# Performance work log

Hardware: AMD Instinct MI355X
Metric: run time of the kernel (lower is better)

The kernel has to match this reference:

```python
import jax, jax.numpy as jnp
import numpy as np

N = 100000      # nodes
E = 3200000     # edges (avg degree 32)
DIN, DH, DOUT = 256, 256, 64
K = 10          # propagation hops


def _uniform(key, shape, fan_in):
    b = 1.0 / np.sqrt(fan_in)
    return jax.random.uniform(key, shape, jnp.float32, -b, b)


def setup_inputs() -> dict:
    key = jax.random.key(0)
    ks = jax.random.split(key, 8)
    x = jax.random.normal(ks[0], (N, DIN), jnp.float32)
    edge_index = jax.random.randint(ks[1], (2, E), 0, N, dtype=jnp.int64)
    W1 = _uniform(ks[2], (DIN, DH), DIN)
    b1 = _uniform(ks[3], (DH,), DIN)
    W2 = _uniform(ks[4], (DH, DOUT), DH)
    b2 = _uniform(ks[5], (DOUT,), DH)
    proj_w = _uniform(ks[6], (DOUT,), DOUT)
    proj_b = _uniform(ks[7], (), DOUT)
    return {"x": x, "edge_index": edge_index, "W1": W1, "b1": b1,
            "W2": W2, "b2": b2, "proj_w": proj_w, "proj_b": proj_b}


def _gcn_norm(edge_index, num_nodes):
    # add self-loops with weight 1, symmetric normalization deg^-1/2 A deg^-1/2
    loops = jnp.arange(num_nodes, dtype=edge_index.dtype)
    row = jnp.concatenate([edge_index[0], loops])
    col = jnp.concatenate([edge_index[1], loops])
    w = jnp.ones(row.shape[0], jnp.float32)
    deg = jax.ops.segment_sum(w, col, num_segments=num_nodes)
    dinv = jnp.where(deg > 0, jax.lax.rsqrt(deg), 0.0)
    norm = dinv[row] * dinv[col]  # edge weight is 1
    return row, col, norm


def reference(x, edge_index, W1, b1, W2, b2, proj_w, proj_b):
    h = jax.nn.relu(x @ W1 + b1)
    h = h @ W2 + b2                               # [N, DOUT]
    row, col, norm = _gcn_norm(edge_index, N)
    preds = [h]
    for _ in range(K):
        h = jax.ops.segment_sum(norm[:, None] * h[row], col, num_segments=N)
        preds.append(h)
    pps = jnp.stack(preds, axis=1)                # [N, K+1, DOUT]
    score = jax.nn.sigmoid(pps @ proj_w + proj_b) # [N, K+1]
    out = jnp.einsum('nk,nkc->nc', score, pps)    # adaptive hop pooling
    return out
```

## Files before the change

kernel.cpp:

```cpp
#include <hip/hip_runtime.h>
#include <hip/hip_bf16.h>
#include <math.h>


#define WAVE 64
#define NBLK 1024

__device__ inline float bf2f(unsigned short u) {
    union { unsigned int i; float f; } v; v.i = ((unsigned int)u) << 16; return v.f;
}
__device__ inline unsigned short f2bf(float f) {
    __hip_bfloat16 b = __float2bfloat16(f);
    union { __hip_bfloat16 b; unsigned short u; } v; v.b = b; return v.u;
}

typedef __attribute__((ext_vector_type(8))) short bf16x8;
typedef __attribute__((ext_vector_type(16))) float f32x16;

__global__ void detect_kernel(const unsigned* __restrict__ e, int* __restrict__ sflag) {
    __shared__ int any;
    if (threadIdx.x == 0) any = 0;
    __syncthreads();
    unsigned nz = 0;
    int t = threadIdx.x;
    for (int i = 0; i < 8; ++i) nz |= e[(size_t)(t * 8 + i) * 2 + 1];
    if (nz) atomicOr(&any, 1);
    __syncthreads();
    if (t == 0) *sflag = any ? 1 : 2;
}

__global__ void passA_kernel(const int* __restrict__ eidx, const int* __restrict__ sflag,
                             int* __restrict__ blk_cnt, int E, int NB, int EPB) {
    __shared__ int lh[512];
    int t = threadIdx.x, blk = blockIdx.x;
    for (int i = t; i < NB; i += 256) lh[i] = 0;
    __syncthreads();
    int s = *sflag;
    int base = blk * EPB;
    int end = base + EPB; if (end > E) end = E;
    for (int e = base + t; e < end; e += 256) {
        int c = eidx[(size_t)s * (size_t)(E + e)];
        atomicAdd(&lh[c >> 8], 1);
    }
    __syncthreads();
    for (int i = t; i < NB; i += 256)
        blk_cnt[(size_t)i * NBLK + blk] = lh[i];
}

__global__ void scan1_kernel(const int* __restrict__ in, int* __restrict__ out,
                             int* __restrict__ bsums, int n) {
    __shared__ int s[256];
    int t = threadIdx.x;
    int idx = blockIdx.x * 1024 + t * 4;
    int x0 = (idx + 0 < n) ? in[idx + 0] : 0;
    int x1 = (idx + 1 < n) ? in[idx + 1] : 0;
    int x2 = (idx + 2 < n) ? in[idx + 2] : 0;
    int x3 = (idx + 3 < n) ? in[idx + 3] : 0;
    int lsum = x0 + x1 + x2 + x3;
    s[t] = lsum;
    __syncthreads();
    for (int o = 1; o < 256; o <<= 1) {
        int v = (t >= o) ? s[t - o] : 0;
        __syncthreads();
        if (t >= o) s[t] += v;
        __syncthreads();
    }
    int excl = s[t] - lsum;
    if (idx + 0 < n) out[idx + 0] = excl;
    if (idx + 1 < n) out[idx + 1] = excl + x0;
    if (idx + 2 < n) out[idx + 2] = excl + x0 + x1;
    if (idx + 3 < n) out[idx + 3] = excl + x0 + x1 + x2;
    if (t == 255) bsums[blockIdx.x] = s[255];
}

__global__ void scan2g_kernel(int* __restrict__ bsums, int nb) {
    __shared__ int part[256];
    int t = threadIdx.x;
    int v[4]; int run = 0;
    #pragma unroll
    for (int j = 0; j < 4; ++j) {
        int i = t * 4 + j;
        int x = (i < nb) ? bsums[i] : 0;
        v[j] = run; run += x;
    }
    part[t] = run;
    __syncthreads();
    for (int o = 1; o < 256; o <<= 1) {
        int x = (t >= o) ? part[t - o] : 0;
        __syncthreads();
        if (t >= o) part[t] += x;
        __syncthreads();
    }
    int excl = part[t] - run;
    #pragma unroll
    for (int j = 0; j < 4; ++j) {
        int i = t * 4 + j;
        if (i < nb) bsums[i] = excl + v[j];
    }
}

__global__ void scan3_kernel(int* __restrict__ arr, const int* __restrict__ bsums,
                             int n, int total) {
    int t = threadIdx.x;
    int idx = blockIdx.x * 1024 + t * 4;
    int add = bsums[blockIdx.x];
    #pragma unroll
    for (int i = 0; i < 4; ++i)
        if (idx + i < n) arr[idx + i] += add;
    if (blockIdx.x == 0 && t == 0) arr[n] = total;
}

__global__ void passB_kernel(const int* __restrict__ eidx, const int* __restrict__ sflag,
                             const int* __restrict__ pbase, int2* __restrict__ pairs,
                             int E, int NB, int EPB) {
    __shared__ int lcur[512];
    int t = threadIdx.x, blk = blockIdx.x;
    for (int i = t; i < NB; i += 256) lcur[i] = pbase[(size_t)i * NBLK + blk];
    __syncthreads();
    int s = *sflag;
    int base = blk * EPB;
    int end = base + EPB; if (end > E) end = E;
    for (int e = base + t; e < end; e += 256) {
        int r = eidx[(size_t)s * (size_t)e];
        int c = eidx[(size_t)s * (size_t)(E + e)];
        int pos = atomicAdd(&lcur[c >> 8], 1);
        pairs[pos] = make_int2(r, c);
    }
}

__global__ void passD_kernel(const int2* __restrict__ pairs, const int* __restrict__ pbase,
                             int* __restrict__ cnt, int N) {
    __shared__ int lcnt[256];
    int b = blockIdx.x, t = threadIdx.x;
    lcnt[t] = 0;
    __syncthreads();
    int w0 = pbase[(size_t)b * NBLK], w1 = pbase[(size_t)(b + 1) * NBLK];
    for (int i = w0 + t; i < w1; i += 256)
        atomicAdd(&lcnt[pairs[i].y & 255], 1);
    __syncthreads();
    int node = b * 256 + t;
    if (node < N) cnt[node] = lcnt[t];
}

__global__ void dinv_kernel(const int* __restrict__ cnt, float* __restrict__ dinv, int n) {
    int i = blockIdx.x * blockDim.x + threadIdx.x;
    if (i < n) dinv[i] = rsqrtf((float)(cnt[i] + 1));
}

__global__ void passC_kernel(const int2* __restrict__ pairs, const int* __restrict__ pbase,
                             const int* __restrict__ offs, int* __restrict__ csr_src,
                             int N) {
    __shared__ int lcur[256];
    int b = blockIdx.x, t = threadIdx.x;
    int node = b * 256 + t;
    lcur[t] = (node < N) ? offs[node] : 0;
    __syncthreads();
    int w0 = pbase[(size_t)b * NBLK], w1 = pbase[(size_t)(b + 1) * NBLK];
    for (int i = w0 + t; i < w1; i += 256) {
        int2 p = pairs[i];
        int pos = atomicAdd(&lcur[p.y & 255], 1);
        csr_src[pos] = p.x;
    }
}

__global__ void wconv_kernel(const float* __restrict__ W, unsigned short* __restrict__ Wt,
                             int K, int Nn) {
    int i = blockIdx.x * blockDim.x + threadIdx.x;
    if (i >= K * Nn) return;
    int n = i / K, k = i - n * K;
    Wt[(size_t)n * K + k] = f2bf(W[(size_t)k * Nn + n]);
}

__global__ __launch_bounds__(256) void gemm1_kernel(
        const float* __restrict__ A, const unsigned short* __restrict__ Bt,
        const float* __restrict__ bias, unsigned short* __restrict__ C, int M) {
    __shared__ unsigned short Asub[128][40];
    __shared__ unsigned short Bsub[256][40];
    int tid = threadIdx.x;
    int wave = tid >> 6, lane = tid & 63;
    int wm = wave >> 1, wn = wave & 1;
    int bm = blockIdx.x * 128;
    int half = lane >> 5, l31 = lane & 31;

    f32x16 acc[2][4] = {};

    for (int k0 = 0; k0 < 256; k0 += 32) {
        #pragma unroll
        for (int i = 0; i < 4; ++i) {
            int f = i * 256 + tid;
            int row = f >> 3, c4 = (f & 7) * 4;
            int grow = bm + row;
            float4 v = make_float4(0.f, 0.f, 0.f, 0.f);
            if (grow < M) v = *(const float4*)(A + (size_t)grow * 256 + k0 + c4);
            ushort4 uu;
            uu.x = f2bf(v.x); uu.y = f2bf(v.y); uu.z = f2bf(v.z); uu.w = f2bf(v.w);
            *(ushort4*)&Asub[row][c4] = uu;
        }
        {
            const unsigned short* p = Bt + (size_t)tid * 256 + k0;
            uint4 u0 = *(const uint4*)(p);
            uint4 u1 = *(const uint4*)(p + 8);
            uint4 u2 = *(const uint4*)(p + 16);
            uint4 u3 = *(const uint4*)(p + 24);
            *(uint4*)&Bsub[tid][0]  = u0;
            *(uint4*)&Bsub[tid][8]  = u1;
            *(uint4*)&Bsub[tid][16] = u2;
            *(uint4*)&Bsub[tid][24] = u3;
        }
        __syncthreads();
        #pragma unroll
        for (int ks = 0; ks < 32; ks += 16) {
            bf16x8 a0 = *(bf16x8*)&Asub[wm * 64 + l31][ks + half * 8];
            bf16x8 a1 = *(bf16x8*)&Asub[wm * 64 + 32 + l31][ks + half * 8];
            #pragma unroll
            for (int j = 0; j < 4; ++j) {
                bf16x8 bf = *(bf16x8*)&Bsub[wn * 128 + j * 32 + l31][ks + half * 8];
                acc[0][j] = __builtin_amdgcn_mfma_f32_32x32x16_bf16(a0, bf, acc[0][j], 0, 0, 0);
                acc[1][j] = __builtin_amdgcn_mfma_f32_32x32x16_bf16(a1, bf, acc[1][j], 0, 0, 0);
            }
        }
        __syncthreads();
    }

    #pragma unroll
    for (int j = 0; j < 4; ++j) {
        int col = wn * 128 + j * 32 + l31;
        float bv = bias[col];
        #pragma unroll
        for (int mt = 0; mt < 2; ++mt) {
            #pragma unroll
            for (int reg = 0; reg < 16; ++reg) {
                int rowin = (reg & 3) + 8 * (reg >> 2) + 4 * half;
                int grow = bm + wm * 64 + mt * 32 + rowin;
                if (grow < M) {
                    float v = fmaxf(acc[mt][j][reg] + bv, 0.f);
                    C[(size_t)grow * 256 + col] = f2bf(v);
                }
            }
        }
    }
}

__global__ __launch_bounds__(256) void gemm2_kernel(
        const unsigned short* __restrict__ A, const unsigned short* __restrict__ Bt,
        const float* __restrict__ bias, float* __restrict__ C, int M) {
    __shared__ unsigned short Asub[128][40];
    __shared__ unsigned short Bsub[64][40];
    int tid = threadIdx.x;
    int wave = tid >> 6, lane = tid & 63;
    int bm = blockIdx.x * 128;
    int half = lane >> 5, l31 = lane & 31;

    f32x16 acc[2] = {};

    for (int k0 = 0; k0 < 256; k0 += 32) {
        #pragma unroll
        for (int i = 0; i < 2; ++i) {
            int f = i * 256 + tid;
            int row = f >> 2, c8 = (f & 3) * 8;
            int grow = bm + row;
            uint4 u = make_uint4(0, 0, 0, 0);
            if (grow < M) u = *(const uint4*)(A + (size_t)grow * 256 + k0 + c8);
            *(uint4*)&Asub[row][c8] = u;
        }
        {
            int n = tid >> 2, k8 = (tid & 3) * 8;
            uint4 u = *(const uint4*)(Bt + (size_t)n * 256 + k0 + k8);
            *(uint4*)&Bsub[n][k8] = u;
        }
        __syncthreads();
        #pragma unroll
        for (int ks = 0; ks < 32; ks += 16) {
            bf16x8 a = *(bf16x8*)&Asub[wave * 32 + l31][ks + half * 8];
            #pragma unroll
            for (int j = 0; j < 2; ++j) {
                bf16x8 bf = *(bf16x8*)&Bsub[j * 32 + l31][ks + half * 8];
                acc[j] = __builtin_amdgcn_mfma_f32_32x32x16_bf16(a, bf, acc[j], 0, 0, 0);
            }
        }
        __syncthreads();
    }

    #pragma unroll
    for (int j = 0; j < 2; ++j) {
        int col = j * 32 + l31;
        float bv = bias[col];
        #pragma unroll
        for (int reg = 0; reg < 16; ++reg) {
            int rowin = (reg & 3) + 8 * (reg >> 2) + 4 * half;
            int grow = bm + wave * 32 + rowin;
            if (grow < M) C[(size_t)grow * 64 + col] = acc[j][reg] + bv;
        }
    }
}

__global__ void hop0_kernel(const float* __restrict__ h, const float* __restrict__ dinv,
                            const float* __restrict__ pw, const float* __restrict__ pb,
                            float* __restrict__ out, __hip_bfloat16* __restrict__ g, int n) {
    int wid = (blockIdx.x * blockDim.x + threadIdx.x) >> 6;
    int lane = threadIdx.x & 63;
    if (wid >= n) return;
    float v = h[(size_t)wid * 64 + lane];
    float d = v * pw[lane];
    #pragma unroll
    for (int o = 32; o > 0; o >>= 1) d += __shfl_xor(d, o, 64);
    float sg = 1.f / (1.f + __expf(-(d + pb[0])));
    out[(size_t)wid * 64 + lane] = sg * v;
    g[(size_t)wid * 64 + lane] = __float2bfloat16(dinv[wid] * v);
}

__global__ void spmm_kernel(const int* __restrict__ offs, const int* __restrict__ src,
                            const float* __restrict__ dinv,
                            const __hip_bfloat16* __restrict__ gin,
                            __hip_bfloat16* __restrict__ gout,
                            float* __restrict__ out,
                            const float* __restrict__ pw, const float* __restrict__ pb,
                            int n) {
    int wid = (blockIdx.x * blockDim.x + threadIdx.x) >> 6;
    int lane = threadIdx.x & 63;
    if (wid >= n) return;
    int c = __builtin_amdgcn_readfirstlane(wid);
    int e = __builtin_amdgcn_readfirstlane(offs[c]);
    int eend = __builtin_amdgcn_readfirstlane(offs[c + 1]);
    float acc = 0.f;
    while (e < eend && (e & 3)) {
        acc += __bfloat162float(gin[(size_t)src[e] * 64 + lane]);
        ++e;
    }
    for (; e + 7 < eend; e += 8) {
        int4 sa = *(const int4*)(src + e);
        int4 sb = *(const int4*)(src + e + 4);
        float v0 = __bfloat162float(gin[(size_t)sa.x * 64 + lane]);
        float v1 = __bfloat162float(gin[(size_t)sa.y * 64 + lane]);
        float v2 = __bfloat162float(gin[(size_t)sa.z * 64 + lane]);
        float v3 = __bfloat162float(gin[(size_t)sa.w * 64 + lane]);
        float v4 = __bfloat162float(gin[(size_t)sb.x * 64 + lane]);
        float v5 = __bfloat162float(gin[(size_t)sb.y * 64 + lane]);
        float v6 = __bfloat162float(gin[(size_t)sb.z * 64 + lane]);
        float v7 = __bfloat162float(gin[(size_t)sb.w * 64 + lane]);
        acc += ((v0 + v1) + (v2 + v3)) + ((v4 + v5) + (v6 + v7));
    }
    for (; e + 3 < eend; e += 4) {
        int4 sa = *(const int4*)(src + e);
        float v0 = __bfloat162float(gin[(size_t)sa.x * 64 + lane]);
        float v1 = __bfloat162float(gin[(size_t)sa.y * 64 + lane]);
        float v2 = __bfloat162float(gin[(size_t)sa.z * 64 + lane]);
        float v3 = __bfloat162float(gin[(size_t)sa.w * 64 + lane]);
        acc += (v0 + v1) + (v2 + v3);
    }
    for (; e < eend; ++e) acc += __bfloat162float(gin[(size_t)src[e] * 64 + lane]);

    float dc = dinv[c];
    float h = dc * (acc + __bfloat162float(gin[(size_t)c * 64 + lane]));
    gout[(size_t)c * 64 + lane] = __float2bfloat16(dc * h);
    float d = h * pw[lane];
    #pragma unroll
    for (int o = 32; o > 0; o >>= 1) d += __shfl_xor(d, o, 64);
    float sg = 1.f / (1.f + __expf(-(d + pb[0])));
    out[(size_t)c * 64 + lane] += sg * h;
}

extern "C" void kernel_launch(void* const* d_in, const int* in_sizes, int n_in,
                              void* d_out, int out_size, void* d_ws, size_t ws_size,
                              hipStream_t stream) {
    const float* x  = (const float*)d_in[0];
    const int* eidx = (const int*)d_in[1];
    const float* W1 = (const float*)d_in[2];
    const float* b1 = (const float*)d_in[3];
    const float* W2 = (const float*)d_in[4];
    const float* b2 = (const float*)d_in[5];
    const float* pw = (const float*)d_in[6];
    const float* pb = (const float*)d_in[7];
    float* out = (float*)d_out;

    const int N = in_sizes[0] / 256;
    const int E = in_sizes[1] / 2;
    const int NB = (N + 255) >> 8;
    const int EPB = (E + NBLK - 1) / NBLK;
    const int M = NB * NBLK;

    size_t woff = 0;
    auto alloc = [&](size_t bytes) -> void* {
        void* p = (char*)d_ws + woff;
        woff += (bytes + 255) & ~(size_t)255;
        return p;
    };
    int*   sflag   = (int*)alloc(4);
    int*   cnt     = (int*)alloc((size_t)N * 4);
    float* dinv    = (float*)alloc((size_t)N * 4);
    int*   offs    = (int*)alloc(((size_t)N + 1) * 4);
    int*   bsums   = (int*)alloc(1024 * 4);
    int*   bsums2  = (int*)alloc(1024 * 4);
    int*   pbase   = (int*)alloc(((size_t)M + 1) * 4);
    int*   csr_src = (int*)alloc((size_t)E * 4);
    int2*  pairs   = (int2*)alloc((size_t)E * 8);
    unsigned short* W1t = (unsigned short*)alloc((size_t)256 * 256 * 2);
    unsigned short* W2t = (unsigned short*)alloc((size_t)64 * 256 * 2);
    const int CH = 50000;
    unsigned short* h1 = (unsigned short*)alloc((size_t)CH * 256 * 2);
    float* hA = (float*)alloc((size_t)N * 64 * 4);
    __hip_bfloat16* gA = (__hip_bfloat16*)alloc((size_t)N * 64 * 2);
    __hip_bfloat16* gB = (__hip_bfloat16*)alloc((size_t)N * 64 * 2);

    detect_kernel<<<1, 256, 0, stream>>>((const unsigned*)eidx, sflag);

    passA_kernel<<<NBLK, 256, 0, stream>>>(eidx, sflag, pbase, E, NB, EPB);
    int nb2 = (M + 1023) / 1024;
    scan1_kernel<<<nb2, 256, 0, stream>>>(pbase, pbase, bsums2, M);
    scan2g_kernel<<<1, 256, 0, stream>>>(bsums2, nb2);
    scan3_kernel<<<nb2, 256, 0, stream>>>(pbase, bsums2, M, E);
    passB_kernel<<<NBLK, 256, 0, stream>>>(eidx, sflag, pbase, pairs, E, NB, EPB);
    passD_kernel<<<NB, 256, 0, stream>>>(pairs, pbase, cnt, N);
    dinv_kernel<<<(N + 255) / 256, 256, 0, stream>>>(cnt, dinv, N);
    int nb1 = (N + 1023) / 1024;
    scan1_kernel<<<nb1, 256, 0, stream>>>(cnt, offs, bsums, N);
    scan2g_kernel<<<1, 256, 0, stream>>>(bsums, nb1);
    scan3_kernel<<<nb1, 256, 0, stream>>>(offs, bsums, N, E);
    passC_kernel<<<NB, 256, 0, stream>>>(pairs, pbase, offs, csr_src, N);

    wconv_kernel<<<(256 * 256 + 255) / 256, 256, 0, stream>>>(W1, W1t, 256, 256);
    wconv_kernel<<<(64 * 256 + 255) / 256, 256, 0, stream>>>(W2, W2t, 256, 64);
    for (int ms = 0; ms < N; ms += CH) {
        int mc = (N - ms < CH) ? (N - ms) : CH;
        int gb = (mc + 127) / 128;
        gemm1_kernel<<<gb, 256, 0, stream>>>(x + (size_t)ms * 256, W1t, b1, h1, mc);
        gemm2_kernel<<<gb, 256, 0, stream>>>(h1, W2t, b2, hA + (size_t)ms * 64, mc);
    }

    int nwb = (N + 3) / 4;
    hop0_kernel<<<nwb, 256, 0, stream>>>(hA, dinv, pw, pb, out, gA, N);
    __hip_bfloat16* gin = gA;
    __hip_bfloat16* gout = gB;
    for (int k = 0; k < 10; ++k) {
        spmm_kernel<<<nwb, 256, 0, stream>>>(offs, csr_src, dinv, gin, gout, out, pw, pb, N);
        __hip_bfloat16* t = gin; gin = gout; gout = t;
    }
}
```

Measured before the change: 1.215 ms.

## Fuse both MLP GEMMs and hop-0 scoring into one kernel with register prefetch

Replaces the chunked gemm1, gemm2 and hop0 launches with one kernel that keeps the 128x256 hidden tile in shared memory in MFMA fragment layout, runs the second GEMM from it, and computes the sigmoid hop-0 score and the scaled bf16 features in the epilogue. This removes the h1 and hA round trips to global memory and several launches. It also prefetches the next x and W1 slice into registers while the current slice is computed. Shared memory use is large (about 100KB), so occupancy is limited to one block per CU, which may cost latency hiding.

```diff
diff --git a/kernel.cpp b/kernel.cpp
--- a/kernel.cpp
+++ b/kernel.cpp
@@ -171,52 +171,95 @@
     Wt[(size_t)n * K + k] = f2bf(W[(size_t)k * Nn + n]);
 }
 
-__global__ __launch_bounds__(256) void gemm1_kernel(
-        const float* __restrict__ A, const unsigned short* __restrict__ Bt,
-        const float* __restrict__ bias, unsigned short* __restrict__ C, int M) {
-    __shared__ unsigned short Asub[128][40];
-    __shared__ unsigned short Bsub[256][40];
+__global__ __launch_bounds__(256, 1) void mlp_fused(
+        const float* __restrict__ x,
+        const unsigned short* __restrict__ W1t,
+        const float* __restrict__ b1,
+        const unsigned short* __restrict__ W2t,
+        const float* __restrict__ b2,
+        const float* __restrict__ dinv,
+        const float* __restrict__ pw, const float* __restrict__ pb,
+        float* __restrict__ out, unsigned short* __restrict__ g,
+        int M) {
+    __shared__ unsigned short xfrag[2][2][128 * 8];
+    __shared__ unsigned short w1frag[2][2][256 * 8];
+    __shared__ unsigned short h1frag[16][2][128 * 8];
+    __shared__ unsigned short w2frag[16][2][64 * 8];
+
     int tid = threadIdx.x;
     int wave = tid >> 6, lane = tid & 63;
+    int half = lane >> 5, l31 = lane & 31;
     int wm = wave >> 1, wn = wave & 1;
     int bm = blockIdx.x * 128;
-    int half = lane >> 5, l31 = lane & 31;
-
-    f32x16 acc[2][4] = {};
-
-    for (int k0 = 0; k0 < 256; k0 += 32) {
+
+    #pragma unroll
+    for (int i = 0; i < 8; ++i) {
+        int F = i * 256 + tid;
+        int s = F >> 7, hf = (F >> 6) & 1, n = F & 63;
+        uint4 u = *(const uint4*)(W2t + (size_t)n * 256 + s * 16 + hf * 8);
+        *(uint4*)&w2frag[s][hf][n * 8] = u;
+    }
+
+    f32x16 acc1[2][4] = {};
+
+    float4 xv[4];
+    uint4 wv[4];
+    #pragma unroll
+    for (int i = 0; i < 4; ++i) {
+        int f = i * 256 + tid;
+        int row = f >> 3, c4 = (f & 7) * 4;
+        int grow = bm + row;
+        xv[i] = (grow < M) ? *(const float4*)(x + (size_t)grow * 256 + c4)
+                           : make_float4(0.f, 0.f, 0.f, 0.f);
+    }
+    {
+        const unsigned short* p = W1t + (size_t)tid * 256;
+        wv[0] = *(const uint4*)(p);
+        wv[1] = *(const uint4*)(p + 8);
+        wv[2] = *(const uint4*)(p + 16);
+        wv[3] = *(const uint4*)(p + 24);
+    }
+
+    for (int it = 0; it < 8; ++it) {
         #pragma unroll
         for (int i = 0; i < 4; ++i) {
             int f = i * 256 + tid;
             int row = f >> 3, c4 = (f & 7) * 4;
-            int grow = bm + row;
-            float4 v = make_float4(0.f, 0.f, 0.f, 0.f);
-            if (grow < M) v = *(const float4*)(A + (size_t)grow * 256 + k0 + c4);
-            ushort4 uu;
-            uu.x = f2bf(v.x); uu.y = f2bf(v.y); uu.z = f2bf(v.z); uu.w = f2bf(v.w);
-            *(ushort4*)&Asub[row][c4] = uu;
-        }
-        {
-            const unsigned short* p = Bt + (size_t)tid * 256 + k0;
-            uint4 u0 = *(const uint4*)(p);
-            uint4 u1 = *(const uint4*)(p + 8);
-            uint4 u2 = *(const uint4*)(p + 16);
-            uint4 u3 = *(const uint4*)(p + 24);
-            *(uint4*)&Bsub[tid][0]  = u0;
-            *(uint4*)&Bsub[tid][8]  = u1;
-            *(uint4*)&Bsub[tid][16] = u2;
-            *(uint4*)&Bsub[tid][24] = u3;
-        }
-        __syncthreads();
+            int k16 = c4 >> 4, hf = (c4 >> 3) & 1, off = c4 & 7;
+            ushort4 u;
+            u.x = f2bf(xv[i].x); u.y = f2bf(xv[i].y);
+            u.z = f2bf(xv[i].z); u.w = f2bf(xv[i].w);
+            *(ushort4*)&xfrag[k16][hf][row * 8 + off] = u;
+        }
         #pragma unroll
-        for (int ks = 0; ks < 32; ks += 16) {
-            bf16x8 a0 = *(bf16x8*)&Asub[wm * 64 + l31][ks + half * 8];
-            bf16x8 a1 = *(bf16x8*)&Asub[wm * 64 + 32 + l31][ks + half * 8];
+        for (int q = 0; q < 4; ++q)
+            *(uint4*)&w1frag[q >> 1][q & 1][tid * 8] = wv[q];
+        __syncthreads();
+        if (it < 7) {
+            int k0 = (it + 1) * 32;
+            #pragma unroll
+            for (int i = 0; i < 4; ++i) {
+                int f = i * 256 + tid;
+                int row = f >> 3, c4 = (f & 7) * 4;
+                int grow = bm + row;
+                xv[i] = (grow < M) ? *(const float4*)(x + (size_t)grow * 256 + k0 + c4)
+                                   : make_float4(0.f, 0.f, 0.f, 0.f);
+            }
+            const unsigned short* p = W1t + (size_t)tid * 256 + k0;
+            wv[0] = *(const uint4*)(p);
+            wv[1] = *(const uint4*)(p + 8);
+            wv[2] = *(const uint4*)(p + 16);
+            wv[3] = *(const uint4*)(p + 24);
+        }
+        #pragma unroll
+        for (int s = 0; s < 2; ++s) {
+            bf16x8 a0 = *(bf16x8*)&xfrag[s][half][(wm * 64 + l31) * 8];
+            bf16x8 a1 = *(bf16x8*)&xfrag[s][half][(wm * 64 + 32 + l31) * 8];
             #pragma unroll
             for (int j = 0; j < 4; ++j) {
-                bf16x8 bf = *(bf16x8*)&Bsub[wn * 128 + j * 32 + l31][ks + half * 8];
-                acc[0][j] = __builtin_amdgcn_mfma_f32_32x32x16_bf16(a0, bf, acc[0][j], 0, 0, 0);
-                acc[1][j] = __builtin_amdgcn_mfma_f32_32x32x16_bf16(a1, bf, acc[1][j], 0, 0, 0);
+                bf16x8 b = *(bf16x8*)&w1frag[s][half][(wn * 128 + j * 32 + l31) * 8];
+                acc1[0][j] = __builtin_amdgcn_mfma_f32_32x32x16_bf16(a0, b, acc1[0][j], 0, 0, 0);
+                acc1[1][j] = __builtin_amdgcn_mfma_f32_32x32x16_bf16(a1, b, acc1[1][j], 0, 0, 0);
             }
         }
         __syncthreads();
@@ -224,89 +267,57 @@
 
     #pragma unroll
     for (int j = 0; j < 4; ++j) {
-        int col = wn * 128 + j * 32 + l31;
-        float bv = bias[col];
+        int ch = wn * 128 + j * 32 + l31;
+        float bb = b1[ch];
+        int k16 = ch >> 4, hf = (ch >> 3) & 1, off = ch & 7;
         #pragma unroll
         for (int mt = 0; mt < 2; ++mt) {
             #pragma unroll
             for (int reg = 0; reg < 16; ++reg) {
                 int rowin = (reg & 3) + 8 * (reg >> 2) + 4 * half;
-                int grow = bm + wm * 64 + mt * 32 + rowin;
-                if (grow < M) {
-                    float v = fmaxf(acc[mt][j][reg] + bv, 0.f);
-                    C[(size_t)grow * 256 + col] = f2bf(v);
-                }
+                int row = wm * 64 + mt * 32 + rowin;
+                float v = fmaxf(acc1[mt][j][reg] + bb, 0.f);
+                h1frag[k16][hf][row * 8 + off] = f2bf(v);
             }
         }
     }
-}
-
-__global__ __launch_bounds__(256) void gemm2_kernel(
-        const unsigned short* __restrict__ A, const unsigned short* __restrict__ Bt,
-        const float* __restrict__ bias, float* __restrict__ C, int M) {
-    __shared__ unsigned short Asub[128][40];
-    __shared__ unsigned short Bsub[64][40];
-    int tid = threadIdx.x;
-    int wave = tid >> 6, lane = tid & 63;
-    int bm = blockIdx.x * 128;
-    int half = lane >> 5, l31 = lane & 31;
-
-    f32x16 acc[2] = {};
-
-    for (int k0 = 0; k0 < 256; k0 += 32) {
+    __syncthreads();
+
+    f32x16 acc2[2] = {};
+    #pragma unroll
+    for (int s = 0; s < 16; ++s) {
+        bf16x8 a = *(bf16x8*)&h1frag[s][half][(wave * 32 + l31) * 8];
         #pragma unroll
-        for (int i = 0; i < 2; ++i) {
-            int f = i * 256 + tid;
-            int row = f >> 2, c8 = (f & 3) * 8;
-            int grow = bm + row;
-            uint4 u = make_uint4(0, 0, 0, 0);
-            if (grow < M) u = *(const uint4*)(A + (size_t)grow * 256 + k0 + c8);
-            *(uint4*)&Asub[row][c8] = u;
-        }
-        {
-            int n = tid >> 2, k8 = (tid & 3) * 8;
-            uint4 u = *(const uint4*)(Bt + (size_t)n * 256 + k0 + k8);
-            *(uint4*)&Bsub[n][k8] = u;
-        }
-        __syncthreads();
-        #pragma unroll
-        for (int ks = 0; ks < 32; ks += 16) {
-            bf16x8 a = *(bf16x8*)&Asub[wave * 32 + l31][ks + half * 8];
-            #pragma unroll
-            for (int j = 0; j < 2; ++j) {
-                bf16x8 bf = *(bf16x8*)&Bsub[j * 32 + l31][ks + half * 8];
-                acc[j] = __builtin_amdgcn_mfma_f32_32x32x16_bf16(a, bf, acc[j], 0, 0, 0);
-            }
-        }
-        __syncthreads();
-    }
-
-    #pragma unroll
-    for (int j = 0; j < 2; ++j) {
-        int col = j * 32 + l31;
-        float bv = bias[col];
-        #pragma unroll
-        for (int reg = 0; reg < 16; ++reg) {
-            int rowin = (reg & 3) + 8 * (reg >> 2) + 4 * half;
-            int grow = bm + wave * 32 + rowin;
-            if (grow < M) C[(size_t)grow * 64 + col] = acc[j][reg] + bv;
-        }
-    }
-}
-
-__global__ void hop0_kernel(const float* __restrict__ h, const float* __restrict__ dinv,
-                            const float* __restrict__ pw, const float* __restrict__ pb,
-                            float* __restrict__ out, __hip_bfloat16* __restrict__ g, int n) {
-    int wid = (blockIdx.x * blockDim.x + threadIdx.x) >> 6;
-    int lane = threadIdx.x & 63;
-    if (wid >= n) return;
-    float v = h[(size_t)wid * 64 + lane];
-    float d = v * pw[lane];
-    #pragma unroll
-    for (int o = 32; o > 0; o >>= 1) d += __shfl_xor(d, o, 64);
-    float sg = 1.f / (1.f + __expf(-(d + pb[0])));
-    out[(size_t)wid * 64 + lane] = sg * v;
-    g[(size_t)wid * 64 + lane] = __float2bfloat16(dinv[wid] * v);
+        for (int j = 0; j < 2; ++j) {
+            bf16x8 b = *(bf16x8*)&w2frag[s][half][(j * 32 + l31) * 8];
+            acc2[j] = __builtin_amdgcn_mfma_f32_32x32x16_bf16(a, b, acc2[j], 0, 0, 0);
+        }
+    }
+
+    float bb0 = b2[l31], bb1 = b2[32 + l31];
+    float pw0 = pw[l31], pw1 = pw[32 + l31];
+    float pbv = pb[0];
+    #pragma unroll
+    for (int reg = 0; reg < 16; ++reg) {
+        int rowin = (reg & 3) + 8 * (reg >> 2) + 4 * half;
+        int row = bm + wave * 32 + rowin;
+        float h0 = acc2[0][reg] + bb0;
+        float h1v = acc2[1][reg] + bb1;
+        float d = h0 * pw0 + h1v * pw1;
+        d += __shfl_xor(d, 1, 64);
+        d += __shfl_xor(d, 2, 64);
+        d += __shfl_xor(d, 4, 64);
+        d += __shfl_xor(d, 8, 64);
+        d += __shfl_xor(d, 16, 64);
+        float sg = 1.f / (1.f + __expf(-(d + pbv)));
+        if (row < M) {
+            float dv = dinv[row];
+            out[(size_t)row * 64 + l31]      = sg * h0;
+            out[(size_t)row * 64 + 32 + l31] = sg * h1v;
+            g[(size_t)row * 64 + l31]        = f2bf(dv * h0);
+            g[(size_t)row * 64 + 32 + l31]   = f2bf(dv * h1v);
+        }
+    }
 }
 
 __global__ void spmm_kernel(const int* __restrict__ offs, const int* __restrict__ src,
@@ -396,9 +407,6 @@
     int2*  pairs   = (int2*)alloc((size_t)E * 8);
     unsigned short* W1t = (unsigned short*)alloc((size_t)256 * 256 * 2);
     unsigned short* W2t = (unsigned short*)alloc((size_t)64 * 256 * 2);
-    const int CH = 50000;
-    unsigned short* h1 = (unsigned short*)alloc((size_t)CH * 256 * 2);
-    float* hA = (float*)alloc((size_t)N * 64 * 4);
     __hip_bfloat16* gA = (__hip_bfloat16*)alloc((size_t)N * 64 * 2);
     __hip_bfloat16* gB = (__hip_bfloat16*)alloc((size_t)N * 64 * 2);
 
@@ -420,15 +428,11 @@
 
     wconv_kernel<<<(256 * 256 + 255) / 256, 256, 0, stream>>>(W1, W1t, 256, 256);
     wconv_kernel<<<(64 * 256 + 255) / 256, 256, 0, stream>>>(W2, W2t, 256, 64);
-    for (int ms = 0; ms < N; ms += CH) {
-        int mc = (N - ms < CH) ? (N - ms) : CH;
-        int gb = (mc + 127) / 128;
-        gemm1_kernel<<<gb, 256, 0, stream>>>(x + (size_t)ms * 256, W1t, b1, h1, mc);
-        gemm2_kernel<<<gb, 256, 0, stream>>>(h1, W2t, b2, hA + (size_t)ms * 64, mc);
-    }
+    int gb = (N + 127) / 128;
+    mlp_fused<<<gb, 256, 0, stream>>>(x, W1t, b1, W2t, b2, dinv, pw, pb,
+                                      out, (unsigned short*)gA, N);
 
     int nwb = (N + 3) / 4;
-    hop0_kernel<<<nwb, 256, 0, stream>>>(hA, dinv, pw, pb, out, gA, N);
     __hip_bfloat16* gin = gA;
     __hip_bfloat16* gout = gB;
     for (int k = 0; k < 10; ++k) {
```

After: 1.150 ms. 1.06x faster.
